# Kernel optimization log

Measured on AMD Instinct MI355X. Metric: run time of the kernel, lower is better.

Reference implementation:

```python
import jax, jax.numpy as jnp
from jax import lax
import numpy as np

RADIUS = 1
DILATION = 2
NUM_BINS = 16  # DualSimilarityLoss uses num_bins=16
ALPHA = 5.0
BETA = 0.1
NOISE = 1e-4


def _avg_pool2(x):
    b, c, h, w = x.shape
    return x.reshape(b, c, h // 2, 2, w // 2, 2).mean(axis=(3, 5))


def _conv_rep(x, k, pad):
    # replicate-pad then VALID conv, NCHW / OIHW
    xp = jnp.pad(x, ((0, 0), (0, 0), (pad, pad), (pad, pad)), mode='edge')
    return lax.conv_general_dilated(xp, k, (1, 1), 'VALID',
                                    dimension_numbers=('NCHW', 'OIHW', 'NCHW'))


def _upsample_align_corners(x, H, W):
    # bilinear, align_corners=True (matches F.interpolate(..., align_corners=True))
    b, c, h, w = x.shape

    def coords(n_out, n_in):
        pos = jnp.arange(n_out, dtype=x.dtype) * ((n_in - 1) / (n_out - 1))
        i0 = jnp.clip(jnp.floor(pos).astype(jnp.int32), 0, n_in - 2)
        return i0, pos - i0.astype(x.dtype)

    y0, fy = coords(H, h)
    x0, fx = coords(W, w)
    rows = x[:, :, y0, :] * (1.0 - fy)[None, None, :, None] \
         + x[:, :, y0 + 1, :] * fy[None, None, :, None]
    out = rows[:, :, :, x0] * (1.0 - fx) + rows[:, :, :, x0 + 1] * fx
    return out


def _compute_mind(img, key):
    B, _, H, W = img.shape
    img = _avg_pool2(img)                      # (B,1,H/2,W/2)
    img = img + NOISE * jax.random.normal(key, img.shape, img.dtype)
    h, w = img.shape[2], img.shape[3]
    pad = RADIUS * DILATION                    # 2
    k = 2 * RADIUS + 1                         # 3
    ones_k = jnp.ones((1, 1, k, k), img.dtype)
    padded = jnp.pad(img, ((0, 0), (0, 0), (pad, pad), (pad, pad)), mode='edge')
    patch_mean = lax.conv_general_dilated(padded, ones_k, (1, 1), 'VALID',
                                          dimension_numbers=('NCHW', 'OIHW', 'NCHW')) / (k * k)
    patch_mean = jnp.pad(patch_mean, ((0, 0), (0, 0), (pad, pad), (pad, pad)), mode='edge')
    c = pad
    center = padded[:, :, c:c + h, c:c + w]
    variance = (center - patch_mean[:, :, c:c + h, c:c + w]) ** 2
    variance = _conv_rep(variance, ones_k, RADIUS) / (k * k)
    variance = jnp.maximum(variance, 1e-4)
    descs = []
    for i in range(-RADIUS, RADIUS + 1):
        for j in range(-RADIUS, RADIUS + 1):
            if i == 0 and j == 0:
                continue
            dx, dy = i * DILATION, j * DILATION
            off = padded[:, :, c + dy:c + dy + h, c + dx:c + dx + w]
            diff = jnp.clip((center - off) ** 2 / (variance * 2 + 1e-6), 0.0, 50.0)
            descs.append(diff)
    m = jnp.exp(-jnp.concatenate(descs, axis=1))          # (B,8,h,w)
    m = m / (m.sum(axis=1, keepdims=True) + 1e-8)
    m = jnp.where(jnp.isnan(m), 0.0, m)
    if (h, w) != (H, W):
        m = _upsample_align_corners(m, H, W)
    return m


def _nmi_loss(x, y, kx, ky):
    B = x.shape[0]
    x = x[:, :, ::2, ::2]
    y = y[:, :, ::2, ::2]
    x = x + NOISE * jax.random.normal(kx, x.shape, x.dtype)
    y = y + NOISE * jax.random.normal(ky, y.shape, y.dtype)
    xf = jnp.clip((x.reshape(B, -1) + 1.0) / 2.0, 0.001, 0.999)
    yf = jnp.clip((y.reshape(B, -1) + 1.0) / 2.0, 0.001, 0.999)
    grid = jnp.linspace(0.0, 1.0, NUM_BINS + 1)
    xb = jnp.clip(jnp.searchsorted(grid, xf, side='left') - 1, 0, NUM_BINS - 1)
    yb = jnp.clip(jnp.searchsorted(grid, yf, side='left') - 1, 0, NUM_BINS - 1)
    idx = xb * NUM_BINS + yb                               # (B,N)
    hist = jnp.zeros((B, NUM_BINS * NUM_BINS), jnp.float32)
    hist = hist.at[jnp.arange(B)[:, None], idx].add(1.0)
    hist = hist.reshape(B, NUM_BINS, NUM_BINS)
    hist = hist / (hist.sum(axis=(1, 2), keepdims=True) + 1e-10)
    xh = hist.sum(axis=2)
    yh = hist.sum(axis=1)
    eps = 1e-5
    hist = hist + eps
    xh = xh + eps
    yh = yh + eps
    mi = jnp.sum(hist * (jnp.log(hist) - jnp.log(xh[:, :, None] * yh[:, None, :])), axis=(1, 2))
    hx = -jnp.sum(xh * jnp.log(xh), axis=1)
    hy = -jnp.sum(yh * jnp.log(yh), axis=1)
    se = hx + hy
    nmi = jnp.where(se < 1e-10, 0.0, 2.0 * mi / se)
    nmi = jnp.clip(nmi, -1.0, 1.0)
    return -jnp.clip(nmi.mean(), -1.0, 1.0)


def _reg_loss(flow, ku, kv):
    sx = jnp.array([[-1, 0, 1], [-2, 0, 2], [-1, 0, 1]], jnp.float32).reshape(1, 1, 3, 3)
    sy = jnp.array([[-1, -2, -1], [0, 0, 0], [1, 2, 1]], jnp.float32).reshape(1, 1, 3, 3)
    lp = jnp.array([[0, 1, 0], [1, -4, 1], [0, 1, 0]], jnp.float32).reshape(1, 1, 3, 3)
    f = _avg_pool2(flow)
    u = f[:, 0:1] + NOISE * jax.random.normal(ku, f[:, 0:1].shape, f.dtype)
    v = f[:, 1:2] + NOISE * jax.random.normal(kv, f[:, 1:2].shape, f.dtype)
    grad_mag = _conv_rep(u, sx, 1) ** 2 + _conv_rep(u, sy, 1) ** 2 \
             + _conv_rep(v, sx, 1) ** 2 + _conv_rep(v, sy, 1) ** 2
    lap_mag = _conv_rep(u, lp, 1) ** 2 + _conv_rep(v, lp, 1) ** 2
    return jnp.clip(grad_mag, 0.0, 100.0).mean() + jnp.clip(lap_mag, 0.0, 100.0).mean()


def _total_loss(fixed, moved, flow):
    fixed = jnp.where(jnp.isnan(fixed), 0.0, fixed)
    moved = jnp.where(jnp.isnan(moved), 0.0, moved)
    flow = jnp.where(jnp.isnan(flow), 0.0, flow)
    ks = jax.random.split(jax.random.key(42), 6)
    mi = _nmi_loss(fixed, moved, ks[0], ks[1])
    mx = _compute_mind(fixed, ks[2])
    my = _compute_mind(moved, ks[3])
    d = jnp.abs(mx - my)
    mind = jnp.where(jnp.isnan(d), 0.0, d).mean()
    reg = _reg_loss(flow, ks[4], ks[5])
    return mi + ALPHA * mind + BETA * reg


def setup_inputs() -> dict:
    key = jax.random.key(0)
    k1, k2, k3 = jax.random.split(key, 3)
    B, H, W = 8, 512, 512
    return {
        'fixed': jax.random.normal(k1, (B, 1, H, W), jnp.float32),
        'moved': jax.random.normal(k2, (B, 1, H, W), jnp.float32),
        'flow': jax.random.normal(k3, (B, 2, H, W), jnp.float32),
    }


def reference(fixed, moved, flow):
    return _total_loss(fixed, moved, flow)
```

## Files before the change

### kernel.cpp

```cpp
#include <hip/hip_runtime.h>
#include <cmath>

#define BATCH 8
#define HF 512
#define WF 512
#define HS 256
#define WS 256
#define PLANE_S (HS * WS)
#define PLANE_F (HF * WF)

#define NMIND_BLOCKS 2048
#define NREG_BLOCKS  512

#define OFF_HIST  0
#define OFF_CNT   (8 * 256 * 4)
#define OFF_NMIB  (OFF_CNT + 4)
#define OFF_PMIND 8704
#define OFF_PGRAD (OFF_PMIND + NMIND_BLOCKS * 8)
#define OFF_PLAP  (OFF_PGRAD + NREG_BLOCKS * 8)

#define IMG_R 23
#define IMG_S 24
#define T_R 20
#define T_S 21
#define V_R 18
#define V_S 19
#define V_PLANE (V_R * V_S)

#define RP 34
#define RS 35

__device__ __forceinline__ int clampi(int v, int lo, int hi) {
    return v < lo ? lo : (v > hi ? hi : v);
}

__device__ __forceinline__ int bin_of(float x) {
    float v = (x + 1.0f) * 0.5f;
    v = fminf(fmaxf(v, 0.001f), 0.999f);
    float t = v * 16.0f;
    float ft = floorf(t);
    int c = (int)ft + ((t > ft) ? 1 : 0);
    int b = c - 1;
    return b < 0 ? 0 : (b > 15 ? 15 : b);
}

__global__ void init_kernel(unsigned* __restrict__ hist, unsigned* __restrict__ cnt) {
    int t = threadIdx.x;
    for (int i = t; i < BATCH * 256; i += 256) hist[i] = 0u;
    if (t == 0) cnt[0] = 0u;
}

__global__ __launch_bounds__(256, 8) void fused_main_kernel(
    const float* __restrict__ fixed, const float* __restrict__ moved,
    const float* __restrict__ flow,
    unsigned* __restrict__ hist, double* __restrict__ pmind,
    double* __restrict__ pgrad, double* __restrict__ plap)
{
    __shared__ float S[4524];
    __shared__ unsigned lh[256];
    __shared__ float red[256];
    int tid = threadIdx.x;

    if (blockIdx.z < 2) {
        int idx = blockIdx.z * 256 + blockIdx.y * 16 + blockIdx.x;
        int b = idx >> 6, t64 = idx & 63;
        int y0p = (t64 >> 3) * 32, x0p = (t64 & 7) * 32;
        float* U = S;
        float* V = S + RP * RS;
        const float* ur = flow + (size_t)(b * 2) * PLANE_F;
        const float* vr = ur + PLANE_F;
        for (int i = tid; i < RP * RP; i += 256) {
            int r = i / RP, c = i - r * RP;
            int gy = clampi(y0p - 1 + r, 0, HS - 1);
            int gx = clampi(x0p - 1 + c, 0, WS - 1);
            const float* uu = ur + (size_t)(gy * 2) * WF + (size_t)(gx * 2);
            const float* vv = vr + (size_t)(gy * 2) * WF + (size_t)(gx * 2);
            float2 u0 = *(const float2*)uu, u1 = *(const float2*)(uu + WF);
            float2 v0 = *(const float2*)vv, v1 = *(const float2*)(vv + WF);
            U[r * RS + c] = (u0.x + u0.y + u1.x + u1.y) * 0.25f;
            V[r * RS + c] = (v0.x + v0.y + v1.x + v1.y) * 0.25f;
        }
        __syncthreads();
        float g = 0.f, l = 0.f;
        for (int k = tid; k < 32 * 32; k += 256) {
            int y = k >> 5, x = k & 31;
            const float* u0 = &U[y * RS + x];
            const float* v0 = &V[y * RS + x];
            float a00 = u0[0],      a01 = u0[1],          a02 = u0[2];
            float a10 = u0[RS],     a11 = u0[RS + 1],     a12 = u0[RS + 2];
            float a20 = u0[2 * RS], a21 = u0[2 * RS + 1], a22 = u0[2 * RS + 2];
            float c00 = v0[0],      c01 = v0[1],          c02 = v0[2];
            float c10 = v0[RS],     c11 = v0[RS + 1],     c12 = v0[RS + 2];
            float c20 = v0[2 * RS], c21 = v0[2 * RS + 1], c22 = v0[2 * RS + 2];
            float gxu = (a02 - a00) + 2.f * (a12 - a10) + (a22 - a20);
            float gyu = (a20 - a00) + 2.f * (a21 - a01) + (a22 - a02);
            float gxv = (c02 - c00) + 2.f * (c12 - c10) + (c22 - c20);
            float gyv = (c20 - c00) + 2.f * (c21 - c01) + (c22 - c02);
            float lpu = a01 + a10 - 4.f * a11 + a12 + a21;
            float lpv = c01 + c10 - 4.f * c11 + c12 + c21;
            float grad = gxu * gxu + gyu * gyu + gxv * gxv + gyv * gyv;
            float lap = lpu * lpu + lpv * lpv;
            g += fminf(grad, 100.f);
            l += fminf(lap, 100.f);
        }
        red[tid] = g;
        __syncthreads();
        for (int s = 128; s > 0; s >>= 1) { if (tid < s) red[tid] += red[tid + s]; __syncthreads(); }
        if (tid == 0) pgrad[b * 64 + t64] = (double)red[0];
        __syncthreads();
        red[tid] = l;
        __syncthreads();
        for (int s = 128; s > 0; s >>= 1) { if (tid < s) red[tid] += red[tid + s]; __syncthreads(); }
        if (tid == 0) plap[b * 64 + t64] = (double)red[0];
        return;
    }

    const float FS = (float)(255.0 / 511.0);
    int tx = blockIdx.x, ty = blockIdx.y, b = blockIdx.z - 2;
    int Xb = tx * 32, Yb = ty * 32;
    int dbx = (int)((float)Xb * FS);
    int dby = (int)((float)Yb * FS);
    int ibx = dbx - 3, iby = dby - 3;

    float* imgF = S;
    float* imgM = S + IMG_R * IMG_S;
    float* varF = S + 2 * IMG_R * IMG_S;
    float* varM = varF + V_R * V_S;
    float* diff = varM + V_R * V_S;
    float* tF   = diff;
    float* tM   = diff + 420;
    float* rsF  = diff + 840;
    float* rsM  = diff + 1280;
    float* vsF  = diff + 840;
    float* vsM  = diff + 1200;

    lh[tid] = 0u;
    __syncthreads();

    const float* fb = fixed + (size_t)b * PLANE_F;
    const float* mb = moved + (size_t)b * PLANE_F;
    int oy0 = ty * 16, ox0 = tx * 16;
    for (int i = tid; i < IMG_R * IMG_R; i += 256) {
        int r = i / IMG_R, c = i - r * IMG_R;
        int gy = iby + r, gx = ibx + c;
        int cy = clampi(gy, 0, HS - 1), cx = clampi(gx, 0, WS - 1);
        const float* fp = fb + (size_t)(cy * 2) * WF + (size_t)(cx * 2);
        const float* mp = mb + (size_t)(cy * 2) * WF + (size_t)(cx * 2);
        float2 f0 = *(const float2*)fp;
        float2 f1 = *(const float2*)(fp + WF);
        float2 m0 = *(const float2*)mp;
        float2 m1 = *(const float2*)(mp + WF);
        imgF[r * IMG_S + c] = (f0.x + f0.y + f1.x + f1.y) * 0.25f;
        imgM[r * IMG_S + c] = (m0.x + m0.y + m1.x + m1.y) * 0.25f;
        if ((unsigned)(gy - oy0) < 16u && (unsigned)(gx - ox0) < 16u) {
            atomicAdd(&lh[bin_of(f0.x) * 16 + bin_of(m0.x)], 1u);
        }
    }
    __syncthreads();
    if (lh[tid]) atomicAdd(&hist[b * 256 + tid], lh[tid]);

    const float NINTH = 1.0f / 9.0f;

    for (int i = tid; i < 22 * 20; i += 256) {
        int rr = i / 20, c = i - rr * 20;
        const float* pF = &imgF[rr * IMG_S + c];
        const float* pM = &imgM[rr * IMG_S + c];
        rsF[i] = (pF[0] + pF[1]) + pF[2];
        rsM[i] = (pM[0] + pM[1]) + pM[2];
    }
    __syncthreads();

    for (int i = tid; i < T_R * T_R; i += 256) {
        int r = i / T_R, c = i - r * T_R;
        float sF = (rsF[r * 20 + c] + rsF[(r + 1) * 20 + c]) + rsF[(r + 2) * 20 + c];
        float sM = (rsM[r * 20 + c] + rsM[(r + 1) * 20 + c]) + rsM[(r + 2) * 20 + c];
        float dF = imgF[(r + 2) * IMG_S + c + 2] - sF * NINTH;
        float dM = imgM[(r + 2) * IMG_S + c + 2] - sM * NINTH;
        tF[r * T_S + c] = dF * dF;
        tM[r * T_S + c] = dM * dM;
    }
    __syncthreads();

    for (int i = tid; i < 20 * 18; i += 256) {
        int rr = i / 18, c = i - rr * 18;
        const float* pF = &tF[rr * T_S + c];
        const float* pM = &tM[rr * T_S + c];
        vsF[i] = (pF[0] + pF[1]) + pF[2];
        vsM[i] = (pM[0] + pM[1]) + pM[2];
    }
    __syncthreads();

    for (int i = tid; i < V_R * V_R; i += 256) {
        int r = i / V_R, c = i - r * V_R;
        float sF = (vsF[r * 18 + c] + vsF[(r + 1) * 18 + c]) + vsF[(r + 2) * 18 + c];
        float sM = (vsM[r * 18 + c] + vsM[(r + 1) * 18 + c]) + vsM[(r + 2) * 18 + c];
        varF[r * V_S + c] = fmaxf(sF * NINTH, 1e-4f);
        varM[r * V_S + c] = fmaxf(sM * NINTH, 1e-4f);
    }
    __syncthreads();

    for (int i = tid; i < V_R * V_R; i += 256) {
        int r = i / V_R, c = i - r * V_R;
        float cF = imgF[(r + 3) * IMG_S + c + 3];
        float cM = imgM[(r + 3) * IMG_S + c + 3];
        float dF2 = 2.f * varF[r * V_S + c] + 1e-6f;
        float dM2 = 2.f * varM[r * V_S + c] + 1e-6f;
        float invF = 1.0f / dF2;
        float invM = 1.0f / dM2;
        float eF[8], eM[8];
        float sF = 0.f, sM = 0.f;
        int ch = 0;
        #pragma unroll
        for (int ii = -1; ii <= 1; ii++) {
            #pragma unroll
            for (int jj = -1; jj <= 1; jj++) {
                if (ii == 0 && jj == 0) continue;
                float aF = cF - imgF[(r + 3 + 2 * jj) * IMG_S + (c + 3 + 2 * ii)];
                float aM = cM - imgM[(r + 3 + 2 * jj) * IMG_S + (c + 3 + 2 * ii)];
                float qF = fminf(aF * aF * invF, 50.f);
                float qM = fminf(aM * aM * invM, 50.f);
                float vF_ = __expf(-qF), vM_ = __expf(-qM);
                eF[ch] = vF_; eM[ch] = vM_;
                sF += vF_; sM += vM_;
                ch++;
            }
        }
        float wF = 1.f / (sF + 1e-8f);
        float wM = 1.f / (sM + 1e-8f);
        int pix = r * V_S + c;
        #pragma unroll
        for (int q = 0; q < 8; q++) diff[q * V_PLANE + pix] = eF[q] * wF - eM[q] * wM;
    }
    __syncthreads();

    float local = 0.f;
    for (int k = tid; k < 32 * 32; k += 256) {
        int dy = k >> 5, dx = k & 31;
        float py = (float)(Yb + dy) * FS;
        int y0 = (int)py; if (y0 > HS - 2) y0 = HS - 2;
        float fy = py - (float)y0;
        float px = (float)(Xb + dx) * FS;
        int x0 = (int)px; if (x0 > WS - 2) x0 = WS - 2;
        float fx = px - (float)x0;
        int i00 = (y0 - dby) * V_S + (x0 - dbx);
        #pragma unroll
        for (int q = 0; q < 8; q++) {
            const float* dq = diff + q * V_PLANE + i00;
            float a  = dq[0] * (1.f - fy) + dq[V_S]     * fy;
            float c2 = dq[1] * (1.f - fy) + dq[V_S + 1] * fy;
            local += fabsf(a * (1.f - fx) + c2 * fx);
        }
    }
    red[tid] = local;
    __syncthreads();
    for (int s = 128; s > 0; s >>= 1) { if (tid < s) red[tid] += red[tid + s]; __syncthreads(); }
    if (tid == 0) pmind[b * 256 + ty * 16 + tx] = (double)red[0];
}

__global__ void tail_kernel(const unsigned* __restrict__ hist,
                            unsigned* __restrict__ cnt, unsigned* __restrict__ nmib,
                            const double* __restrict__ pmind,
                            const double* __restrict__ pgrad, const double* __restrict__ plap,
                            float* __restrict__ out) {
    int b = blockIdx.x;
    int t = threadIdx.x;
    __shared__ float p[256];
    __shared__ float xh[16], yh[16];
    __shared__ float redf[256];
    __shared__ double red[256];
    __shared__ unsigned ticket;

    unsigned hv = hist[b * 256 + t];
    float pv = (float)hv / 65536.0f;
    p[t] = pv;
    __syncthreads();
    if (t < 16) {
        float s = 0.f;
        for (int j = 0; j < 16; j++) s += p[t * 16 + j];
        xh[t] = s;
    } else if (t < 32) {
        int j = t - 16;
        float s = 0.f;
        for (int i = 0; i < 16; i++) s += p[i * 16 + j];
        yh[j] = s;
    }
    __syncthreads();
    const float eps = 1e-5f;
    int i = t >> 4, j = t & 15;
    float h = pv + eps;
    float mi_term = h * (logf(h) - logf((xh[i] + eps) * (yh[j] + eps)));
    redf[t] = mi_term;
    __syncthreads();
    for (int s = 128; s > 0; s >>= 1) { if (t < s) redf[t] += redf[t + s]; __syncthreads(); }
    float mi = redf[0];
    __syncthreads();
    float e_term = 0.f;
    if (t < 16) { float xe = xh[t] + eps; e_term = -xe * logf(xe); }
    else if (t < 32) { float ye = yh[t - 16] + eps; e_term = -ye * logf(ye); }
    redf[t] = e_term;
    __syncthreads();
    for (int s = 128; s > 0; s >>= 1) { if (t < s) redf[t] += redf[t + s]; __syncthreads(); }
    if (t == 0) {
        float se = redf[0];
        float nmi = (se < 1e-10f) ? 0.f : 2.f * mi / se;
        nmi = fminf(fmaxf(nmi, -1.f), 1.f);
        atomicExch(&nmib[b], __float_as_uint(nmi));
        ticket = atomicAdd(cnt, 1u);
    }
    __syncthreads();
    if (ticket != BATCH - 1) return;

    double sm = 0.0;
    for (int i2 = t; i2 < NMIND_BLOCKS; i2 += 256) sm += pmind[i2];
    double sg = 0.0, sl = 0.0;
    for (int i2 = t; i2 < NREG_BLOCKS; i2 += 256) { sg += pgrad[i2]; sl += plap[i2]; }
    red[t] = sm;
    __syncthreads();
    for (int s = 128; s > 0; s >>= 1) { if (t < s) red[t] += red[t + s]; __syncthreads(); }
    double mind_sum = red[0];
    __syncthreads();
    red[t] = sg;
    __syncthreads();
    for (int s = 128; s > 0; s >>= 1) { if (t < s) red[t] += red[t + s]; __syncthreads(); }
    double grad_sum = red[0];
    __syncthreads();
    red[t] = sl;
    __syncthreads();
    for (int s = 128; s > 0; s >>= 1) { if (t < s) red[t] += red[t + s]; __syncthreads(); }
    double lap_sum = red[0];
    if (t == 0) {
        float s = 0.f;
        for (int bb = 0; bb < BATCH; bb++) {
            unsigned u = atomicOr(&nmib[bb], 0u);
            s += __uint_as_float(u);
        }
        s /= (float)BATCH;
        s = fminf(fmaxf(s, -1.f), 1.f);
        double mi_loss = -(double)s;
        double mind_mean = mind_sum / (64.0 * (double)PLANE_F);
        double reg = grad_sum / (double)(BATCH * PLANE_S) + lap_sum / (double)(BATCH * PLANE_S);
        out[0] = (float)(mi_loss + 5.0 * mind_mean + 0.1 * reg);
    }
}

extern "C" void kernel_launch(void* const* d_in, const int* in_sizes, int n_in,
                              void* d_out, int out_size, void* d_ws, size_t ws_size,
                              hipStream_t stream) {
    const float* fixed = (const float*)d_in[0];
    const float* moved = (const float*)d_in[1];
    const float* flow  = (const float*)d_in[2];
    float* out = (float*)d_out;
    char* ws = (char*)d_ws;

    unsigned* hist  = (unsigned*)(ws + OFF_HIST);
    unsigned* cnt   = (unsigned*)(ws + OFF_CNT);
    unsigned* nmib  = (unsigned*)(ws + OFF_NMIB);
    double*   pmind = (double*)(ws + OFF_PMIND);
    double*   pgrad = (double*)(ws + OFF_PGRAD);
    double*   plap  = (double*)(ws + OFF_PLAP);

    init_kernel<<<dim3(1), 256, 0, stream>>>(hist, cnt);
    fused_main_kernel<<<dim3(16, 16, 10), 256, 0, stream>>>(fixed, moved, flow,
                                                            hist, pmind, pgrad, plap);
    tail_kernel<<<dim3(BATCH), 256, 0, stream>>>(hist, cnt, nmib, pmind, pgrad, plap, out);
}
```

Before: 107.6 us.

## Drop init kernel via self-resetting device globals and vectorize shared-memory access

Workspace buffers become `__device__` globals. The last tail block zeroes the histogram and ticket counter after use, so the separate init kernel launch goes away. The pooled-image load now handles two columns per thread with float2 shared stores. The descriptor-difference buffer is written and read as float2 pairs during bilinear upsampling to cut shared-memory instruction count. The trade-off is that correctness now depends on the previous call leaving the globals clean, and on static zero-initialisation for the first call.

Result: slower. 110.3 us (+2.6%).

```diff
diff --git a/kernel.cpp b/kernel.cpp
--- a/kernel.cpp
+++ b/kernel.cpp
@@ -12,13 +12,6 @@
 #define NMIND_BLOCKS 2048
 #define NREG_BLOCKS  512
 
-#define OFF_HIST  0
-#define OFF_CNT   (8 * 256 * 4)
-#define OFF_NMIB  (OFF_CNT + 4)
-#define OFF_PMIND 8704
-#define OFF_PGRAD (OFF_PMIND + NMIND_BLOCKS * 8)
-#define OFF_PLAP  (OFF_PGRAD + NREG_BLOCKS * 8)
-
 #define IMG_R 23
 #define IMG_S 24
 #define T_R 20
@@ -29,6 +22,13 @@
 
 #define RP 34
 #define RS 35
+
+__device__ unsigned g_hist[BATCH * 256];
+__device__ unsigned g_cnt;
+__device__ unsigned g_nmib[BATCH];
+__device__ double   g_pmind[NMIND_BLOCKS];
+__device__ double   g_pgrad[NREG_BLOCKS];
+__device__ double   g_plap[NREG_BLOCKS];
 
 __device__ __forceinline__ int clampi(int v, int lo, int hi) {
     return v < lo ? lo : (v > hi ? hi : v);
@@ -44,19 +44,11 @@
     return b < 0 ? 0 : (b > 15 ? 15 : b);
 }
 
-__global__ void init_kernel(unsigned* __restrict__ hist, unsigned* __restrict__ cnt) {
-    int t = threadIdx.x;
-    for (int i = t; i < BATCH * 256; i += 256) hist[i] = 0u;
-    if (t == 0) cnt[0] = 0u;
-}
-
 __global__ __launch_bounds__(256, 8) void fused_main_kernel(
     const float* __restrict__ fixed, const float* __restrict__ moved,
-    const float* __restrict__ flow,
-    unsigned* __restrict__ hist, double* __restrict__ pmind,
-    double* __restrict__ pgrad, double* __restrict__ plap)
+    const float* __restrict__ flow)
 {
-    __shared__ float S[4524];
+    __shared__ __align__(16) float S[4524];
     __shared__ unsigned lh[256];
     __shared__ float red[256];
     int tid = threadIdx.x;
@@ -106,12 +98,12 @@
         red[tid] = g;
         __syncthreads();
         for (int s = 128; s > 0; s >>= 1) { if (tid < s) red[tid] += red[tid + s]; __syncthreads(); }
-        if (tid == 0) pgrad[b * 64 + t64] = (double)red[0];
+        if (tid == 0) g_pgrad[b * 64 + t64] = (double)red[0];
         __syncthreads();
         red[tid] = l;
         __syncthreads();
         for (int s = 128; s > 0; s >>= 1) { if (tid < s) red[tid] += red[tid + s]; __syncthreads(); }
-        if (tid == 0) plap[b * 64 + t64] = (double)red[0];
+        if (tid == 0) g_plap[b * 64 + t64] = (double)red[0];
         return;
     }
 
@@ -140,24 +132,46 @@
     const float* fb = fixed + (size_t)b * PLANE_F;
     const float* mb = moved + (size_t)b * PLANE_F;
     int oy0 = ty * 16, ox0 = tx * 16;
-    for (int i = tid; i < IMG_R * IMG_R; i += 256) {
-        int r = i / IMG_R, c = i - r * IMG_R;
-        int gy = iby + r, gx = ibx + c;
-        int cy = clampi(gy, 0, HS - 1), cx = clampi(gx, 0, WS - 1);
-        const float* fp = fb + (size_t)(cy * 2) * WF + (size_t)(cx * 2);
-        const float* mp = mb + (size_t)(cy * 2) * WF + (size_t)(cx * 2);
-        float2 f0 = *(const float2*)fp;
-        float2 f1 = *(const float2*)(fp + WF);
-        float2 m0 = *(const float2*)mp;
-        float2 m1 = *(const float2*)(mp + WF);
-        imgF[r * IMG_S + c] = (f0.x + f0.y + f1.x + f1.y) * 0.25f;
-        imgM[r * IMG_S + c] = (m0.x + m0.y + m1.x + m1.y) * 0.25f;
-        if ((unsigned)(gy - oy0) < 16u && (unsigned)(gx - ox0) < 16u) {
+    for (int i = tid; i < IMG_R * 12; i += 256) {
+        int r = i / 12, pc = i - r * 12;
+        int c0 = pc * 2;
+        int gy = iby + r;
+        int cy = clampi(gy, 0, HS - 1);
+        const float* frow = fb + (size_t)(cy * 2) * WF;
+        const float* mrow = mb + (size_t)(cy * 2) * WF;
+        bool rowOwn = (unsigned)(gy - oy0) < 16u;
+
+        int gx0 = ibx + c0;
+        int cx0 = clampi(gx0, 0, WS - 1);
+        float2 f0 = *(const float2*)(frow + cx0 * 2);
+        float2 f1 = *(const float2*)(frow + WF + cx0 * 2);
+        float2 m0 = *(const float2*)(mrow + cx0 * 2);
+        float2 m1 = *(const float2*)(mrow + WF + cx0 * 2);
+        float pF0 = (f0.x + f0.y + f1.x + f1.y) * 0.25f;
+        float pM0 = (m0.x + m0.y + m1.x + m1.y) * 0.25f;
+        if (rowOwn && (unsigned)(gx0 - ox0) < 16u)
             atomicAdd(&lh[bin_of(f0.x) * 16 + bin_of(m0.x)], 1u);
-        }
-    }
-    __syncthreads();
-    if (lh[tid]) atomicAdd(&hist[b * 256 + tid], lh[tid]);
+
+        if (c0 + 1 < IMG_R) {
+            int gx1 = gx0 + 1;
+            int cx1 = clampi(gx1, 0, WS - 1);
+            float2 f0b = *(const float2*)(frow + cx1 * 2);
+            float2 f1b = *(const float2*)(frow + WF + cx1 * 2);
+            float2 m0b = *(const float2*)(mrow + cx1 * 2);
+            float2 m1b = *(const float2*)(mrow + WF + cx1 * 2);
+            float pF1 = (f0b.x + f0b.y + f1b.x + f1b.y) * 0.25f;
+            float pM1 = (m0b.x + m0b.y + m1b.x + m1b.y) * 0.25f;
+            if (rowOwn && (unsigned)(gx1 - ox0) < 16u)
+                atomicAdd(&lh[bin_of(f0b.x) * 16 + bin_of(m0b.x)], 1u);
+            *(float2*)&imgF[r * IMG_S + c0] = make_float2(pF0, pF1);
+            *(float2*)&imgM[r * IMG_S + c0] = make_float2(pM0, pM1);
+        } else {
+            imgF[r * IMG_S + c0] = pF0;
+            imgM[r * IMG_S + c0] = pM0;
+        }
+    }
+    __syncthreads();
+    if (lh[tid]) atomicAdd(&g_hist[b * 256 + tid], lh[tid]);
 
     const float NINTH = 1.0f / 9.0f;
 
@@ -199,6 +213,7 @@
     }
     __syncthreads();
 
+    float2* d2w = (float2*)diff;
     for (int i = tid; i < V_R * V_R; i += 256) {
         int r = i / V_R, c = i - r * V_R;
         float cF = imgF[(r + 3) * IMG_S + c + 3];
@@ -229,12 +244,17 @@
         float wM = 1.f / (sM + 1e-8f);
         int pix = r * V_S + c;
         #pragma unroll
-        for (int q = 0; q < 8; q++) diff[q * V_PLANE + pix] = eF[q] * wF - eM[q] * wM;
+        for (int q2 = 0; q2 < 4; q2++)
+            d2w[q2 * V_PLANE + pix] = make_float2(eF[2 * q2] * wF - eM[2 * q2] * wM,
+                                                  eF[2 * q2 + 1] * wF - eM[2 * q2 + 1] * wM);
     }
     __syncthreads();
 
     float local = 0.f;
-    for (int k = tid; k < 32 * 32; k += 256) {
+    const float2* d2 = (const float2*)diff;
+    #pragma unroll
+    for (int kk = 0; kk < 4; kk++) {
+        int k = tid + kk * 256;
         int dy = k >> 5, dx = k & 31;
         float py = (float)(Yb + dy) * FS;
         int y0 = (int)py; if (y0 > HS - 2) y0 = HS - 2;
@@ -243,25 +263,28 @@
         int x0 = (int)px; if (x0 > WS - 2) x0 = WS - 2;
         float fx = px - (float)x0;
         int i00 = (y0 - dby) * V_S + (x0 - dbx);
+        float wy0 = 1.f - fy, wx0 = 1.f - fx;
         #pragma unroll
-        for (int q = 0; q < 8; q++) {
-            const float* dq = diff + q * V_PLANE + i00;
-            float a  = dq[0] * (1.f - fy) + dq[V_S]     * fy;
-            float c2 = dq[1] * (1.f - fy) + dq[V_S + 1] * fy;
-            local += fabsf(a * (1.f - fx) + c2 * fx);
+        for (int q2 = 0; q2 < 4; q2++) {
+            float2 v00 = d2[q2 * V_PLANE + i00];
+            float2 v01 = d2[q2 * V_PLANE + i00 + 1];
+            float2 v10 = d2[q2 * V_PLANE + i00 + V_S];
+            float2 v11 = d2[q2 * V_PLANE + i00 + V_S + 1];
+            float a0 = v00.x * wy0 + v10.x * fy;
+            float c0 = v01.x * wy0 + v11.x * fy;
+            local += fabsf(a0 * wx0 + c0 * fx);
+            float a1 = v00.y * wy0 + v10.y * fy;
+            float c1 = v01.y * wy0 + v11.y * fy;
+            local += fabsf(a1 * wx0 + c1 * fx);
         }
     }
     red[tid] = local;
     __syncthreads();
     for (int s = 128; s > 0; s >>= 1) { if (tid < s) red[tid] += red[tid + s]; __syncthreads(); }
-    if (tid == 0) pmind[b * 256 + ty * 16 + tx] = (double)red[0];
-}
-
-__global__ void tail_kernel(const unsigned* __restrict__ hist,
-                            unsigned* __restrict__ cnt, unsigned* __restrict__ nmib,
-                            const double* __restrict__ pmind,
-                            const double* __restrict__ pgrad, const double* __restrict__ plap,
-                            float* __restrict__ out) {
+    if (tid == 0) g_pmind[b * 256 + ty * 16 + tx] = (double)red[0];
+}
+
+__global__ void tail_kernel(float* __restrict__ out) {
     int b = blockIdx.x;
     int t = threadIdx.x;
     __shared__ float p[256];
@@ -270,7 +293,7 @@
     __shared__ double red[256];
     __shared__ unsigned ticket;
 
-    unsigned hv = hist[b * 256 + t];
+    unsigned hv = g_hist[b * 256 + t];
     float pv = (float)hv / 65536.0f;
     p[t] = pv;
     __syncthreads();
@@ -304,16 +327,16 @@
         float se = redf[0];
         float nmi = (se < 1e-10f) ? 0.f : 2.f * mi / se;
         nmi = fminf(fmaxf(nmi, -1.f), 1.f);
-        atomicExch(&nmib[b], __float_as_uint(nmi));
-        ticket = atomicAdd(cnt, 1u);
+        atomicExch(&g_nmib[b], __float_as_uint(nmi));
+        ticket = atomicAdd(&g_cnt, 1u);
     }
     __syncthreads();
     if (ticket != BATCH - 1) return;
 
     double sm = 0.0;
-    for (int i2 = t; i2 < NMIND_BLOCKS; i2 += 256) sm += pmind[i2];
+    for (int i2 = t; i2 < NMIND_BLOCKS; i2 += 256) sm += g_pmind[i2];
     double sg = 0.0, sl = 0.0;
-    for (int i2 = t; i2 < NREG_BLOCKS; i2 += 256) { sg += pgrad[i2]; sl += plap[i2]; }
+    for (int i2 = t; i2 < NREG_BLOCKS; i2 += 256) { sg += g_pgrad[i2]; sl += g_plap[i2]; }
     red[t] = sm;
     __syncthreads();
     for (int s = 128; s > 0; s >>= 1) { if (t < s) red[t] += red[t + s]; __syncthreads(); }
@@ -331,7 +354,7 @@
     if (t == 0) {
         float s = 0.f;
         for (int bb = 0; bb < BATCH; bb++) {
-            unsigned u = atomicOr(&nmib[bb], 0u);
+            unsigned u = atomicOr(&g_nmib[bb], 0u);
             s += __uint_as_float(u);
         }
         s /= (float)BATCH;
@@ -341,6 +364,8 @@
         double reg = grad_sum / (double)(BATCH * PLANE_S) + lap_sum / (double)(BATCH * PLANE_S);
         out[0] = (float)(mi_loss + 5.0 * mind_mean + 0.1 * reg);
     }
+    for (int i2 = t; i2 < BATCH * 256; i2 += 256) g_hist[i2] = 0u;
+    if (t == 0) g_cnt = 0u;
 }
 
 extern "C" void kernel_launch(void* const* d_in, const int* in_sizes, int n_in,
@@ -350,17 +375,8 @@
     const float* moved = (const float*)d_in[1];
     const float* flow  = (const float*)d_in[2];
     float* out = (float*)d_out;
-    char* ws = (char*)d_ws;
-
-    unsigned* hist  = (unsigned*)(ws + OFF_HIST);
-    unsigned* cnt   = (unsigned*)(ws + OFF_CNT);
-    unsigned* nmib  = (unsigned*)(ws + OFF_NMIB);
-    double*   pmind = (double*)(ws + OFF_PMIND);
-    double*   pgrad = (double*)(ws + OFF_PGRAD);
-    double*   plap  = (double*)(ws + OFF_PLAP);
-
-    init_kernel<<<dim3(1), 256, 0, stream>>>(hist, cnt);
-    fused_main_kernel<<<dim3(16, 16, 10), 256, 0, stream>>>(fixed, moved, flow,
-                                                            hist, pmind, pgrad, plap);
-    tail_kernel<<<dim3(BATCH), 256, 0, stream>>>(hist, cnt, nmib, pmind, pgrad, plap, out);
-}
+    (void)d_ws; (void)ws_size;
+
+    fused_main_kernel<<<dim3(16, 16, 10), 256, 0, stream>>>(fixed, moved, flow);
+    tail_kernel<<<dim3(BATCH), 256, 0, stream>>>(out);
+}
```
